# Kernel tuning notes

Hardware: AMD Instinct MI355X
Metric: run time of the kernel (lower is better)

Reference implementation:

```python
import jax, jax.numpy as jnp
import numpy as np

GRID = 0.5          # voxel spacing (Angstrom)
NG = 48             # voxels per axis
VDW_O = 1.52        # vdw radius of water oxygen
MULTI = 1.5         # mask radius multiplier
WEIGHT = 25.0       # channel-1 'on' weight
N_ATOMS = 1024
CHUNK = 128         # atoms processed per scan step (bounds peak memory)


def setup_inputs() -> dict:
    key = jax.random.key(0)
    # water oxygen coordinates uniformly in the 24A grid box
    vecs = jax.random.uniform(key, (N_ATOMS, 3), dtype=jnp.float32) * (GRID * NG)
    return {"vecs": vecs}


def _chunk_counts(v, xs, r2):
    # v: [C,3] atom coords; xs: [G] voxel coords (grid*index)
    d2ax = (v[:, :, None] - xs[None, None, :]) ** 2            # [C,3,G]
    d2 = (d2ax[:, 0, :, None, None]
          + d2ax[:, 1, None, :, None]
          + d2ax[:, 2, None, None, :])                          # [C,G,G,G]
    # strict inequality matches torch.where(d < multi*r, 1, 0); sqrt is monotone
    return jnp.sum((d2 < r2).astype(jnp.float32), axis=0)       # [G,G,G]


def reference(vecs):
    xs = GRID * jnp.arange(NG, dtype=jnp.float32)               # voxel coords
    r2 = jnp.float32((MULTI * VDW_O) ** 2)
    vchunks = vecs.reshape(N_ATOMS // CHUNK, CHUNK, 3)

    def body(acc, v):
        return acc + _chunk_counts(v, xs, r2), None

    counts, _ = jax.lax.scan(body, jnp.zeros((NG, NG, NG), jnp.float32), vchunks)
    # channel 0 and channel 1 both hold the atom-coverage count before masking
    cond = counts >= 0.9
    ch0 = jnp.where(cond, jnp.float32(1.0), jnp.float32(0.0))
    ch1 = jnp.where(cond, jnp.float32(WEIGHT), jnp.float32(1.0))
    return jnp.stack([ch0, ch1], axis=0)                        # [2,G,G,G]
```

## Files before the change

### kernel.cpp

```cpp
#include <hip/hip_runtime.h>

#define NG   48
#define NG2  (NG * NG)
#define NG3  (NG * NG * NG)
#define N_ATOMS 1024

__device__ __forceinline__ float radius2_f32() {
    const double rd = 1.5 * 1.52;
    return (float)(rd * rd);
}

__global__ void wat_init_out(float* __restrict__ out) {
    int i = blockIdx.x * blockDim.x + threadIdx.x;
    const int n4 = (2 * NG3) / 4;
    if (i < n4) {
        float v = (i < NG3 / 4) ? 0.0f : 1.0f;
        reinterpret_cast<float4*>(out)[i] = make_float4(v, v, v, v);
    }
}

__global__ void wat_scatter(const float* __restrict__ vecs,
                            float* __restrict__ out) {
    const int a = blockIdx.x;
    const float ax = vecs[3 * a + 0];
    const float ay = vecs[3 * a + 1];
    const float az = vecs[3 * a + 2];

    const float R2 = radius2_f32();
    const float Rc = 2.2805f;

    int x0 = max(0,      (int)floorf((ax - Rc) * 2.0f));
    int x1 = min(NG - 1, (int)ceilf ((ax + Rc) * 2.0f));
    int y0 = max(0,      (int)floorf((ay - Rc) * 2.0f));
    int y1 = min(NG - 1, (int)ceilf ((ay + Rc) * 2.0f));
    int z0 = max(0,      (int)floorf((az - Rc) * 2.0f));
    int z1 = min(NG - 1, (int)ceilf ((az + Rc) * 2.0f));

    const int nx = x1 - x0 + 1;
    const int ny = y1 - y0 + 1;
    const int nz = z1 - z0 + 1;
    const int total = nx * ny * nz;

    for (int t = threadIdx.x; t < total; t += blockDim.x) {
        const int iz  = z0 + (t % nz);
        const int rem = t / nz;
        const int iy  = y0 + (rem % ny);
        const int ix  = x0 + (rem / ny);

        const float dx = __fsub_rn(ax, 0.5f * (float)ix);
        const float dy = __fsub_rn(ay, 0.5f * (float)iy);
        const float dz = __fsub_rn(az, 0.5f * (float)iz);
        const float d2 = __fadd_rn(__fadd_rn(__fmul_rn(dx, dx),
                                             __fmul_rn(dy, dy)),
                                   __fmul_rn(dz, dz));
        if (d2 < R2) {
            const int idx = ix * NG2 + iy * NG + iz;
            out[idx]       = 1.0f;
            out[NG3 + idx] = 25.0f;
        }
    }
}

extern "C" void kernel_launch(void* const* d_in, const int* in_sizes, int n_in,
                              void* d_out, int out_size, void* d_ws, size_t ws_size,
                              hipStream_t stream) {
    const float* vecs = (const float*)d_in[0];
    float* out = (float*)d_out;

    wat_init_out<<<216, 256, 0, stream>>>(out);
    wat_scatter<<<N_ATOMS, 256, 0, stream>>>(vecs, out);
}
```

Baseline: 57.30 us.

## Replace init+scatter with fused gather kernel using per-tile atom culling

Replaces the two-kernel scheme (fill output, then per-atom scatter writes) with a single gather kernel. Each 8x8x8 voxel tile first culls atoms to a shared-memory candidate list by bounding box, then each voxel tests the candidates with early exit and writes both channels once. This removes a kernel launch, the redundant init writes and the scattered duplicate stores. In exchange, each block reads all atom coordinates, and the candidate list is built with shared atomics.

```diff
diff --git a/kernel.cpp b/kernel.cpp
--- a/kernel.cpp
+++ b/kernel.cpp
@@ -5,60 +5,68 @@
 #define NG3  (NG * NG * NG)
 #define N_ATOMS 1024
 
-__device__ __forceinline__ float radius2_f32() {
+__global__ __launch_bounds__(512) void wat_fused(const float* __restrict__ vecs,
+                                                 float* __restrict__ out) {
+    __shared__ float cx[N_ATOMS], cy[N_ATOMS], cz[N_ATOMS];
+    __shared__ int ncand;
+
+    const int t = threadIdx.x;
+    if (t == 0) ncand = 0;
+    __syncthreads();
+
+    const int bx0 = blockIdx.x * 8;
+    const int by0 = blockIdx.y * 8;
+    const int bz0 = blockIdx.z * 8;
+
+    const float margin = 2.2805f;
+    const float lox = 0.5f * (float)bx0 - margin;
+    const float hix = 0.5f * (float)(bx0 + 7) + margin;
+    const float loy = 0.5f * (float)by0 - margin;
+    const float hiy = 0.5f * (float)(by0 + 7) + margin;
+    const float loz = 0.5f * (float)bz0 - margin;
+    const float hiz = 0.5f * (float)(bz0 + 7) + margin;
+
+    for (int a = t; a < N_ATOMS; a += 512) {
+        const float ax = vecs[3 * a + 0];
+        const float ay = vecs[3 * a + 1];
+        const float az = vecs[3 * a + 2];
+        if (ax >= lox && ax <= hix &&
+            ay >= loy && ay <= hiy &&
+            az >= loz && az <= hiz) {
+            const int p = atomicAdd(&ncand, 1);
+            cx[p] = ax; cy[p] = ay; cz[p] = az;
+        }
+    }
+    __syncthreads();
+    const int n = ncand;
+
+    const int lz = t & 7;
+    const int ly = (t >> 3) & 7;
+    const int lx = t >> 6;
+    const int ix = bx0 + lx;
+    const int iy = by0 + ly;
+    const int iz = bz0 + lz;
+    const float vx = 0.5f * (float)ix;
+    const float vy = 0.5f * (float)iy;
+    const float vz = 0.5f * (float)iz;
+
     const double rd = 1.5 * 1.52;
-    return (float)(rd * rd);
-}
+    const float R2 = (float)(rd * rd);
 
-__global__ void wat_init_out(float* __restrict__ out) {
-    int i = blockIdx.x * blockDim.x + threadIdx.x;
-    const int n4 = (2 * NG3) / 4;
-    if (i < n4) {
-        float v = (i < NG3 / 4) ? 0.0f : 1.0f;
-        reinterpret_cast<float4*>(out)[i] = make_float4(v, v, v, v);
-    }
-}
-
-__global__ void wat_scatter(const float* __restrict__ vecs,
-                            float* __restrict__ out) {
-    const int a = blockIdx.x;
-    const float ax = vecs[3 * a + 0];
-    const float ay = vecs[3 * a + 1];
-    const float az = vecs[3 * a + 2];
-
-    const float R2 = radius2_f32();
-    const float Rc = 2.2805f;
-
-    int x0 = max(0,      (int)floorf((ax - Rc) * 2.0f));
-    int x1 = min(NG - 1, (int)ceilf ((ax + Rc) * 2.0f));
-    int y0 = max(0,      (int)floorf((ay - Rc) * 2.0f));
-    int y1 = min(NG - 1, (int)ceilf ((ay + Rc) * 2.0f));
-    int z0 = max(0,      (int)floorf((az - Rc) * 2.0f));
-    int z1 = min(NG - 1, (int)ceilf ((az + Rc) * 2.0f));
-
-    const int nx = x1 - x0 + 1;
-    const int ny = y1 - y0 + 1;
-    const int nz = z1 - z0 + 1;
-    const int total = nx * ny * nz;
-
-    for (int t = threadIdx.x; t < total; t += blockDim.x) {
-        const int iz  = z0 + (t % nz);
-        const int rem = t / nz;
-        const int iy  = y0 + (rem % ny);
-        const int ix  = x0 + (rem / ny);
-
-        const float dx = __fsub_rn(ax, 0.5f * (float)ix);
-        const float dy = __fsub_rn(ay, 0.5f * (float)iy);
-        const float dz = __fsub_rn(az, 0.5f * (float)iz);
+    bool covered = false;
+    for (int i = 0; i < n; ++i) {
+        const float dx = __fsub_rn(cx[i], vx);
+        const float dy = __fsub_rn(cy[i], vy);
+        const float dz = __fsub_rn(cz[i], vz);
         const float d2 = __fadd_rn(__fadd_rn(__fmul_rn(dx, dx),
                                              __fmul_rn(dy, dy)),
                                    __fmul_rn(dz, dz));
-        if (d2 < R2) {
-            const int idx = ix * NG2 + iy * NG + iz;
-            out[idx]       = 1.0f;
-            out[NG3 + idx] = 25.0f;
-        }
+        if (d2 < R2) { covered = true; break; }
     }
+
+    const int idx = ix * NG2 + iy * NG + iz;
+    out[idx]       = covered ? 1.0f  : 0.0f;
+    out[NG3 + idx] = covered ? 25.0f : 1.0f;
 }
 
 extern "C" void kernel_launch(void* const* d_in, const int* in_sizes, int n_in,
@@ -67,6 +75,6 @@
     const float* vecs = (const float*)d_in[0];
     float* out = (float*)d_out;
 
-    wat_init_out<<<216, 256, 0, stream>>>(out);
-    wat_scatter<<<N_ATOMS, 256, 0, stream>>>(vecs, out);
+    dim3 grid(NG / 8, NG / 8, NG / 8);
+    wat_fused<<<grid, 512, 0, stream>>>(vecs, out);
 }
```

Result: slower. 58.75 us (+2.5%).
